# Optimization experiments

Hardware: AMD Instinct MI355X
Metric: run time of the kernel (lower is better)

## Reference

```python
import jax, jax.numpy as jnp
import numpy as np

N_NODES = 100000
N_EDGES = 1600000
IN_F = 128
OUT_F = 32
HEADS = 4
NEG_SLOPE = 0.2
EPS = 1e-8


def setup_inputs() -> dict:
    key = jax.random.key(0)
    k1, k2, k3, k4 = jax.random.split(key, 4)
    x = jax.random.normal(k1, (N_NODES, IN_F), dtype=jnp.float32)
    # torch Linear weight layout: [out_features*num_heads, in_features]
    # xavier_uniform-like scale
    limW = float(np.sqrt(6.0 / (IN_F + OUT_F * HEADS)))
    W = jax.random.uniform(k2, (OUT_F * HEADS, IN_F), dtype=jnp.float32, minval=-limW, maxval=limW)
    lima = float(np.sqrt(6.0 / (HEADS + 2 * OUT_F)))
    a = jax.random.uniform(k3, (HEADS, 2 * OUT_F), dtype=jnp.float32, minval=-lima, maxval=lima)
    edge_index = jax.random.randint(k4, (2, N_EDGES), 0, N_NODES, dtype=jnp.int64)
    return {"x": x, "W": W, "a": a, "edge_index": edge_index}


def reference(x, W, a, edge_index):
    # x: [N, in], W: [H*F, in], a: [H, 2F], edge_index: [2, E]
    N = x.shape[0]
    H = HEADS
    F = OUT_F
    h = (x @ W.T).reshape(N, H, F)                      # [N, H, F]
    src, dst = edge_index[0], edge_index[1]
    h_src = h[src]                                       # [E, H, F]
    h_dst = h[dst]                                       # [E, H, F]
    # (cat([h_src, h_dst], -1) * a).sum(-1) == h_src@a_src + h_dst@a_dst
    a_src, a_dst = a[:, :F], a[:, F:]
    att = jnp.einsum('ehf,hf->eh', h_src, a_src) + jnp.einsum('ehf,hf->eh', h_dst, a_dst)  # [E, H]
    att = jnp.where(att >= 0, att, NEG_SLOPE * att)      # leaky_relu(0.2)
    att = jnp.exp(att - att.max())                       # global-max stabilization (as in source)
    att_sum = jax.ops.segment_sum(att, dst, num_segments=N)    # [N, H]
    att = att / (att_sum[dst] + EPS)                     # segment softmax
    # dropout is identity in eval mode
    out = jax.ops.segment_sum(att[..., None] * h_src, dst, num_segments=N)  # [N, H, F]
    return out.reshape(N, H * F)                         # concat=True
```

## Files before the change

kernel.cpp:

```cpp
#include <hip/hip_runtime.h>
#include <hip/hip_bf16.h>

#define NEG_SLOPE 0.2f
#define EPSV 1e-8f
#define BCAP 10240

typedef float f32x4 __attribute__((ext_vector_type(4)));
typedef short bf16x8 __attribute__((ext_vector_type(8)));
typedef unsigned short us8 __attribute__((ext_vector_type(8)));

static __device__ __forceinline__ float bf16tof(unsigned short s) {
    union { unsigned u; float f; } c; c.u = ((unsigned)s) << 16; return c.f;
}
static __device__ __forceinline__ unsigned short ftobf16(float f) {
    __hip_bfloat16 b = __float2bfloat16(f);
    return *(unsigned short*)&b;
}
static __device__ __forceinline__ float leaky_exp(float v) {
    v = fmaxf(v, NEG_SLOPE * v);
    return __expf(v);
}

__global__ __launch_bounds__(256, 2) void k_gemm(
        const float* __restrict__ x, const float* __restrict__ W,
        const float* __restrict__ a, unsigned short* __restrict__ h_bf,
        float* __restrict__ asrc, float* __restrict__ adst, int N) {
    __shared__ unsigned short xs[128 * 128];
    __shared__ unsigned short ws[128 * 128];
    __shared__ float sa[256];
    int tid = threadIdx.x;
    int nb = blockIdx.x * 128;

    sa[tid] = a[tid];

#pragma unroll
    for (int it = 0; it < 16; ++it) {
        int f = tid + 256 * it;
        int row = f >> 5;
        int k0 = (f & 31) << 2;
        int sw = row * 128 + (k0 ^ ((row & 7) << 3));
        int n = nb + row; if (n >= N) n = N - 1;
        float4 v = *(const float4*)(x + (size_t)n * 128 + k0);
        ushort4 o;
        o.x = ftobf16(v.x); o.y = ftobf16(v.y);
        o.z = ftobf16(v.z); o.w = ftobf16(v.w);
        *(ushort4*)&xs[sw] = o;
        float4 wv = *(const float4*)(W + (size_t)row * 128 + k0);
        ushort4 ow;
        ow.x = ftobf16(wv.x); ow.y = ftobf16(wv.y);
        ow.z = ftobf16(wv.z); ow.w = ftobf16(wv.w);
        *(ushort4*)&ws[sw] = ow;
    }
    __syncthreads();

    int w  = tid >> 6;
    int l  = tid & 63;
    int lr = l & 15;
    int lg = l >> 4;

    f32x4 acc[2][8];
    {
        f32x4 zz = {0.f, 0.f, 0.f, 0.f};
#pragma unroll
        for (int nt = 0; nt < 2; ++nt)
#pragma unroll
            for (int jt = 0; jt < 8; ++jt)
                acc[nt][jt] = zz;
    }

#pragma unroll
    for (int ks = 0; ks < 4; ++ks) {
        int kofs = ks * 32 + lg * 8;
        bf16x8 xf[2];
#pragma unroll
        for (int nt = 0; nt < 2; ++nt) {
            int row = w * 32 + nt * 16 + lr;
            xf[nt] = *(const bf16x8*)&xs[row * 128 + (kofs ^ ((row & 7) << 3))];
        }
#pragma unroll
        for (int jt = 0; jt < 8; ++jt) {
            int j = jt * 16 + lr;
            bf16x8 wf = *(const bf16x8*)&ws[j * 128 + (kofs ^ ((j & 7) << 3))];
#pragma unroll
            for (int nt = 0; nt < 2; ++nt)
                acc[nt][jt] = __builtin_amdgcn_mfma_f32_16x16x32_bf16(
                    wf, xf[nt], acc[nt][jt], 0, 0, 0);
        }
    }

#pragma unroll
    for (int g = 0; g < 4; ++g) {
        f32x4 as0 = *(const f32x4*)&sa[g * 64 +      lg * 4];
        f32x4 as1 = *(const f32x4*)&sa[g * 64 + 16 + lg * 4];
        f32x4 ad0 = *(const f32x4*)&sa[g * 64 + 32 + lg * 4];
        f32x4 ad1 = *(const f32x4*)&sa[g * 64 + 48 + lg * 4];
#pragma unroll
        for (int nt = 0; nt < 2; ++nt) {
            float ps = 0.f, pd = 0.f;
#pragma unroll
            for (int r = 0; r < 4; ++r) {
                ps += acc[nt][2 * g][r] * as0[r] + acc[nt][2 * g + 1][r] * as1[r];
                pd += acc[nt][2 * g][r] * ad0[r] + acc[nt][2 * g + 1][r] * ad1[r];
            }
            ps += __shfl_xor(ps, 16); pd += __shfl_xor(pd, 16);
            ps += __shfl_xor(ps, 32); pd += __shfl_xor(pd, 32);
            if (lg == 0) {
                int n = nb + w * 32 + nt * 16 + lr;
                if (n < N) {
                    asrc[(size_t)n * 4 + g] = ps;
                    adst[(size_t)n * 4 + g] = pd;
                }
            }
        }
    }

    __syncthreads();
#pragma unroll
    for (int nt = 0; nt < 2; ++nt) {
        int row = w * 32 + nt * 16 + lr;
        int m = (row & 7) << 3;
#pragma unroll
        for (int jt = 0; jt < 8; ++jt) {
            int j0 = jt * 16 + lg * 4;
            ushort4 o;
            o.x = ftobf16(acc[nt][jt][0]);
            o.y = ftobf16(acc[nt][jt][1]);
            o.z = ftobf16(acc[nt][jt][2]);
            o.w = ftobf16(acc[nt][jt][3]);
            *(ushort4*)&xs[row * 128 + (j0 ^ m)] = o;
        }
    }
    __syncthreads();
#pragma unroll
    for (int it = 0; it < 8; ++it) {
        int f = tid + 256 * it;
        int row = f >> 4;
        int c8 = (f & 15) << 3;
        int n = nb + row;
        if (n < N) {
            us8 v = *(const us8*)&xs[row * 128 + (c8 ^ ((row & 7) << 3))];
            *(us8*)(h_bf + (size_t)n * 128 + c8) = v;
        }
    }
}

__global__ __launch_bounds__(256) void k_bscatter(const int* __restrict__ ei,
        int* __restrict__ relcur, unsigned* __restrict__ ebuf, int E, int epb) {
    __shared__ int hist[256];
    __shared__ int wcur[256];
    __shared__ int bslot[256];
    int t = threadIdx.x;
    int lo = blockIdx.x * epb;
    int hi = min(E, lo + epb);
    hist[t] = 0;
    wcur[t] = 0;
    __syncthreads();
    int sreg[8], dreg[8];
    int cnt = 0;
#pragma unroll
    for (int k = 0; k < 8; k++) {
        int e = lo + t + 256 * k;
        if (e < hi) {
            sreg[k] = ei[e];
            dreg[k] = ei[E + e];
            atomicAdd(&hist[dreg[k] >> 9], 1);
            cnt = k + 1;
        }
    }
    __syncthreads();
    int c = hist[t];
    int res = c ? atomicAdd(&relcur[t], c) : 0;
    bslot[t] = t * BCAP + res;
    __syncthreads();
    for (int k = 0; k < cnt; k++) {
        int s = sreg[k];
        int d = dreg[k];
        int b = d >> 9;
        int off = atomicAdd(&wcur[b], 1);
        int slot = bslot[b] + off;
        if (slot < (b + 1) * BCAP)
            ebuf[slot] = ((unsigned)(d & 511) << 23) | (unsigned)s;
    }
}

__global__ __launch_bounds__(256) void k_bscan(const int* __restrict__ relcur,
                                               int* __restrict__ gbase,
                                               int* __restrict__ row_ptr,
                                               int NBK, int N, int E) {
    __shared__ int sm[256];
    int t = threadIdx.x;
    int c = (t < NBK) ? min(relcur[t], BCAP) : 0;
    sm[t] = c;
    __syncthreads();
    for (int off = 1; off < 256; off <<= 1) {
        int u = (t >= off) ? sm[t - off] : 0;
        __syncthreads();
        sm[t] += u;
        __syncthreads();
    }
    gbase[t] = sm[t] - c;
    if (t == 0) row_ptr[N] = E;
}

__global__ __launch_bounds__(256) void k_build(const int* __restrict__ relcur,
        const int* __restrict__ gbase, const unsigned* __restrict__ ebuf,
        int* __restrict__ row_ptr, int* __restrict__ csr_src, int N) {
    __shared__ int hist[512];
    __shared__ int excl[512];
    __shared__ int sm[256];
    int b = blockIdx.x;
    int t = threadIdx.x;
    int cnt = min(relcur[b], BCAP);
    int base = gbase[b];
    int d0 = b << 9;
    const unsigned* ep = ebuf + (size_t)b * BCAP;

    hist[t] = 0; hist[t + 256] = 0;
    __syncthreads();
    for (int i = t; i < cnt; i += 256)
        atomicAdd(&hist[ep[i] >> 23], 1);
    __syncthreads();

    int a0 = hist[2 * t], a1 = hist[2 * t + 1];
    int s = a0 + a1;
    sm[t] = s;
    __syncthreads();
    for (int off = 1; off < 256; off <<= 1) {
        int u = (t >= off) ? sm[t - off] : 0;
        __syncthreads();
        sm[t] += u;
        __syncthreads();
    }
    int ex = sm[t] - s;
    excl[2 * t] = ex;
    excl[2 * t + 1] = ex + a0;
    int n0 = d0 + 2 * t, n1 = d0 + 2 * t + 1;
    if (n0 < N) row_ptr[n0] = base + ex;
    if (n1 < N) row_ptr[n1] = base + ex + a0;
    __syncthreads();

    for (int i = t; i < cnt; i += 256) {
        unsigned p = ep[i];
        int pos = base + atomicAdd(&excl[p >> 23], 1);
        csr_src[pos] = (int)(p & 0x7FFFFFu);
    }
}

__global__ __launch_bounds__(256) void k_agg(
        const int* __restrict__ row_ptr, const int* __restrict__ csr_src,
        const float* __restrict__ asrc, const float* __restrict__ adst,
        const unsigned short* __restrict__ h_bf,
        float* __restrict__ out, int N) {
    __shared__ int   se[4][68];
    __shared__ float sw[4][272];
    int tid = threadIdx.x;
    int w  = tid >> 6;
    int l  = tid & 63;
    int gg = l >> 4;
    int m  = l & 15;
    int hh = m >> 2;

    int n = blockIdx.x * 16 + w * 4 + gg;
    bool valid = (n < N);
    int nc = valid ? n : (N - 1);
    int lo  = row_ptr[nc];
    int deg = row_ptr[nc + 1] - lo;
    float4 dv = *(const float4*)(adst + 4 * (size_t)nc);

    int md = deg;
    md = max(md, __shfl_xor(md, 16));
    md = max(md, __shfl_xor(md, 32));

    float acc[8] = {};
    float asum = 0.f;
    const unsigned short* hp = h_bf + 8 * m;

#define ACC8(U, WT) do { \
        union { unsigned u; float f; } q; \
        q.u = (U).x << 16;         acc[0] += (WT) * q.f; \
        q.u = (U).x & 0xFFFF0000u; acc[1] += (WT) * q.f; \
        q.u = (U).y << 16;         acc[2] += (WT) * q.f; \
        q.u = (U).y & 0xFFFF0000u; acc[3] += (WT) * q.f; \
        q.u = (U).z << 16;         acc[4] += (WT) * q.f; \
        q.u = (U).z & 0xFFFF0000u; acc[5] += (WT) * q.f; \
        q.u = (U).w << 16;         acc[6] += (WT) * q.f; \
        q.u = (U).w & 0xFFFF0000u; acc[7] += (WT) * q.f; \
    } while (0)

    for (int base = 0; base < md; base += 16) {
        int e = base + m;
        if (e < deg) {
            int s = csr_src[lo + e];
            se[w][17 * gg + m] = s;
            float4 sv = *(const float4*)(asrc + 4 * (size_t)s);
            float4 wv;
            wv.x = leaky_exp(sv.x + dv.x);
            wv.y = leaky_exp(sv.y + dv.y);
            wv.z = leaky_exp(sv.z + dv.z);
            wv.w = leaky_exp(sv.w + dv.w);
            *(float4*)&sw[w][68 * gg + 4 * m] = wv;
        }
        __builtin_amdgcn_wave_barrier();
        int cnt = min(deg - base, 16);
        int i = 0;
        for (; i + 4 <= cnt; i += 4) {
            int s0 = se[w][17 * gg + i];
            int s1 = se[w][17 * gg + i + 1];
            int s2 = se[w][17 * gg + i + 2];
            int s3 = se[w][17 * gg + i + 3];
            float w0 = sw[w][68 * gg + 4 * i + hh];
            float w1 = sw[w][68 * gg + 4 * i + 4 + hh];
            float w2 = sw[w][68 * gg + 4 * i + 8 + hh];
            float w3 = sw[w][68 * gg + 4 * i + 12 + hh];
            uint4 u0 = *(const uint4*)(hp + (size_t)s0 * 128);
            uint4 u1 = *(const uint4*)(hp + (size_t)s1 * 128);
            uint4 u2 = *(const uint4*)(hp + (size_t)s2 * 128);
            uint4 u3 = *(const uint4*)(hp + (size_t)s3 * 128);
            ACC8(u0, w0);
            ACC8(u1, w1);
            ACC8(u2, w2);
            ACC8(u3, w3);
            asum += (w0 + w1) + (w2 + w3);
        }
        for (; i < cnt; i++) {
            int s0 = se[w][17 * gg + i];
            float w0 = sw[w][68 * gg + 4 * i + hh];
            uint4 u0 = *(const uint4*)(hp + (size_t)s0 * 128);
            ACC8(u0, w0);
            asum += w0;
        }
        __builtin_amdgcn_wave_barrier();
    }
#undef ACC8

    if (valid) {
        float inv = 1.f / (asum + EPSV);
        float4 o0, o1;
        o0.x = acc[0] * inv; o0.y = acc[1] * inv;
        o0.z = acc[2] * inv; o0.w = acc[3] * inv;
        o1.x = acc[4] * inv; o1.y = acc[5] * inv;
        o1.z = acc[6] * inv; o1.w = acc[7] * inv;
        *(float4*)(out + (size_t)n * 128 + 8 * m) = o0;
        *(float4*)(out + (size_t)n * 128 + 8 * m + 4) = o1;
    }
}

extern "C" void kernel_launch(void* const* d_in, const int* in_sizes, int n_in,
                              void* d_out, int out_size, void* d_ws, size_t ws_size,
                              hipStream_t stream) {
    const float* x = (const float*)d_in[0];
    const float* W = (const float*)d_in[1];
    const float* a = (const float*)d_in[2];
    const int* ei = (const int*)d_in[3];
    float* out = (float*)d_out;

    int N = in_sizes[0] / 128;
    int E = in_sizes[3] / 2;
    int NBK = (N + 511) >> 9;

    char* wsb = (char*)d_ws;
    size_t off = 0;
    auto alloc = [&](size_t bytes) -> void* {
        void* p = wsb + off;
        off += (bytes + 255) / 256 * 256;
        return p;
    };
    unsigned short* h_bf = (unsigned short*)alloc((size_t)N * 128 * 2);
    float* asrc = (float*)alloc((size_t)N * 4 * 4);
    float* adst = (float*)alloc((size_t)N * 4 * 4);
    int* row_ptr = (int*)alloc((size_t)(N + 1) * 4);
    int* relcur = (int*)alloc(256 * 4);
    int* gbase = (int*)alloc(256 * 4);
    unsigned* ebuf = (unsigned*)alloc((size_t)NBK * BCAP * 4);
    int* csr_src = (int*)alloc((size_t)E * 4);

    hipMemsetAsync(relcur, 0, 256 * 4, stream);

    dim3 ggrid((N + 127) / 128);
    k_gemm<<<ggrid, 256, 0, stream>>>(x, W, a, h_bf, asrc, adst, N);
    int nsb = (E + 2047) / 2048;
    k_bscatter<<<nsb, 256, 0, stream>>>(ei, relcur, ebuf, E, 2048);
    k_bscan<<<1, 256, 0, stream>>>(relcur, gbase, row_ptr, NBK, N, E);
    k_build<<<NBK, 256, 0, stream>>>(relcur, gbase, ebuf, row_ptr, csr_src, N);
    k_agg<<<(N + 15) / 16, 256, 0, stream>>>(row_ptr, csr_src, asrc, adst, h_bf, out, N);
}
```

Measured before the change: 238.0 us.

## Double-buffer edge metadata and software-pipeline gathers in aggregation kernel

Splits the per-wave shared edge buffers into two halves so the next chunk's csr_src index and asrc attention load are issued before the current chunk's gathers and committed to shared memory afterwards. The inner gather loop becomes a rolling two-deep prefetch of bf16 feature rows instead of four independent loads per iteration. The aim is to hide global-load latency across chunk boundaries and inside the loop. In exchange it doubles shared-memory use, keeps more values live in registers, and lowers the number of gathers in flight per iteration from four to two, which may reduce memory-level parallelism.

```diff
diff --git a/kernel.cpp b/kernel.cpp
--- a/kernel.cpp
+++ b/kernel.cpp
@@ -251,8 +251,8 @@
         const float* __restrict__ asrc, const float* __restrict__ adst,
         const unsigned short* __restrict__ h_bf,
         float* __restrict__ out, int N) {
-    __shared__ int   se[4][68];
-    __shared__ float sw[4][272];
+    __shared__ int   se[4][2][68];
+    __shared__ float sw[4][2][272];
     int tid = threadIdx.x;
     int w  = tid >> 6;
     int l  = tid & 63;
@@ -270,6 +270,7 @@
     int md = deg;
     md = max(md, __shfl_xor(md, 16));
     md = max(md, __shfl_xor(md, 32));
+    int nch = (md + 15) >> 4;
 
     float acc[8] = {};
     float asum = 0.f;
@@ -287,47 +288,73 @@
         q.u = (U).w & 0xFFFF0000u; acc[7] += (WT) * q.f; \
     } while (0)
 
-    for (int base = 0; base < md; base += 16) {
-        int e = base + m;
-        if (e < deg) {
-            int s = csr_src[lo + e];
-            se[w][17 * gg + m] = s;
-            float4 sv = *(const float4*)(asrc + 4 * (size_t)s);
-            float4 wv;
-            wv.x = leaky_exp(sv.x + dv.x);
-            wv.y = leaky_exp(sv.y + dv.y);
-            wv.z = leaky_exp(sv.z + dv.z);
-            wv.w = leaky_exp(sv.w + dv.w);
-            *(float4*)&sw[w][68 * gg + 4 * m] = wv;
+    if (m < deg) {
+        int s = csr_src[lo + m];
+        se[w][0][17 * gg + m] = s;
+        float4 sv = *(const float4*)(asrc + 4 * (size_t)s);
+        float4 wv;
+        wv.x = leaky_exp(sv.x + dv.x);
+        wv.y = leaky_exp(sv.y + dv.y);
+        wv.z = leaky_exp(sv.z + dv.z);
+        wv.w = leaky_exp(sv.w + dv.w);
+        *(float4*)&sw[w][0][68 * gg + 4 * m] = wv;
+    }
+
+    for (int c = 0; c < nch; ++c) {
+        int cb = c & 1;
+        int sN = 0; float4 svN; bool haveN = false;
+        {
+            int eN = (c + 1) * 16 + m;
+            if (c + 1 < nch && eN < deg) {
+                sN = csr_src[lo + eN];
+                svN = *(const float4*)(asrc + 4 * (size_t)sN);
+                haveN = true;
+            }
         }
         __builtin_amdgcn_wave_barrier();
-        int cnt = min(deg - base, 16);
+        int base16 = c * 16;
+        int cnt = min(deg - base16, 16);
+        const int*   sep = &se[w][cb][17 * gg];
+        const float* swp = &sw[w][cb][68 * gg];
         int i = 0;
-        for (; i + 4 <= cnt; i += 4) {
-            int s0 = se[w][17 * gg + i];
-            int s1 = se[w][17 * gg + i + 1];
-            int s2 = se[w][17 * gg + i + 2];
-            int s3 = se[w][17 * gg + i + 3];
-            float w0 = sw[w][68 * gg + 4 * i + hh];
-            float w1 = sw[w][68 * gg + 4 * i + 4 + hh];
-            float w2 = sw[w][68 * gg + 4 * i + 8 + hh];
-            float w3 = sw[w][68 * gg + 4 * i + 12 + hh];
-            uint4 u0 = *(const uint4*)(hp + (size_t)s0 * 128);
-            uint4 u1 = *(const uint4*)(hp + (size_t)s1 * 128);
-            uint4 u2 = *(const uint4*)(hp + (size_t)s2 * 128);
-            uint4 u3 = *(const uint4*)(hp + (size_t)s3 * 128);
+        uint4 u0, u1;
+        if (cnt >= 2) {
+            u0 = *(const uint4*)(hp + (size_t)sep[0] * 128);
+            u1 = *(const uint4*)(hp + (size_t)sep[1] * 128);
+        }
+        for (; i + 4 <= cnt; i += 2) {
+            uint4 t0 = *(const uint4*)(hp + (size_t)sep[i + 2] * 128);
+            uint4 t1 = *(const uint4*)(hp + (size_t)sep[i + 3] * 128);
+            float w0 = swp[4 * i + hh];
+            float w1 = swp[4 * i + 4 + hh];
             ACC8(u0, w0);
             ACC8(u1, w1);
-            ACC8(u2, w2);
-            ACC8(u3, w3);
-            asum += (w0 + w1) + (w2 + w3);
-        }
-        for (; i < cnt; i++) {
-            int s0 = se[w][17 * gg + i];
-            float w0 = sw[w][68 * gg + 4 * i + hh];
-            uint4 u0 = *(const uint4*)(hp + (size_t)s0 * 128);
+            asum += w0 + w1;
+            u0 = t0; u1 = t1;
+        }
+        if (i + 2 <= cnt) {
+            float w0 = swp[4 * i + hh];
+            float w1 = swp[4 * i + 4 + hh];
             ACC8(u0, w0);
+            ACC8(u1, w1);
+            asum += w0 + w1;
+            i += 2;
+        }
+        for (; i < cnt; ++i) {
+            int s0 = sep[i];
+            float w0 = swp[4 * i + hh];
+            uint4 uu = *(const uint4*)(hp + (size_t)s0 * 128);
+            ACC8(uu, w0);
             asum += w0;
+        }
+        if (haveN) {
+            se[w][cb ^ 1][17 * gg + m] = sN;
+            float4 wv;
+            wv.x = leaky_exp(svN.x + dv.x);
+            wv.y = leaky_exp(svN.y + dv.y);
+            wv.z = leaky_exp(svN.z + dv.z);
+            wv.w = leaky_exp(svN.w + dv.w);
+            *(float4*)&sw[w][cb ^ 1][68 * gg + 4 * m] = wv;
         }
         __builtin_amdgcn_wave_barrier();
     }
```

Result: no change. 235.6 us (-1.0%).
